# Kernel tuning notes

Hardware: AMD Instinct MI355X
Metric: run time of the kernel (lower is better)

## Reference

```python
import jax, jax.numpy as jnp
import numpy as np

BBOX_XFORM_CLIP = float(np.log(1000.0 / 16.0))
WX, WY, WW, WH = 10.0, 10.0, 5.0, 5.0  # torchvision default box-coder weights


def setup_inputs() -> dict:
    key = jax.random.key(0)
    B, P, C, E = 8, 25000, 81, 256
    H, W = 800, 800
    k1, k2, k3, k4, k5 = jax.random.split(key, 5)
    N = B * P
    class_logits = jax.random.normal(k1, (N, C), dtype=jnp.float32)
    box_regression = jax.random.normal(k2, (N, C * 4), dtype=jnp.float32) * 0.1
    id_embedding = jax.random.normal(k3, (N, E), dtype=jnp.float32)
    # valid proposals: x1<x2, y1<y2, inside the image
    xy = jax.random.uniform(k4, (B, P, 2), dtype=jnp.float32) * (W - 65.0)
    wh = jax.random.uniform(k5, (B, P, 2), dtype=jnp.float32) * 63.0 + 1.0
    proposals = jnp.concatenate([xy, xy + wh], axis=-1)  # [B,P,4] x1,y1,x2,y2
    return {
        'class_logits': class_logits,
        'box_regression': box_regression,
        'id_embedding': id_embedding,
        'proposals': proposals,
        'img_h': H,
        'img_w': W,
    }


def _decode_boxes(box_regression, proposals_flat):
    # torchvision BoxCoder.decode, vectorized. proposals_flat: [N,4]
    N = proposals_flat.shape[0]
    C = box_regression.shape[1] // 4
    deltas = box_regression.reshape(N, C, 4)
    x1, y1, x2, y2 = jnp.split(proposals_flat, 4, axis=-1)  # each [N,1]
    w = x2 - x1
    h = y2 - y1
    cx = x1 + 0.5 * w
    cy = y1 + 0.5 * h
    dx = deltas[..., 0] / WX  # [N,C]
    dy = deltas[..., 1] / WY
    dw = jnp.minimum(deltas[..., 2] / WW, BBOX_XFORM_CLIP)
    dh = jnp.minimum(deltas[..., 3] / WH, BBOX_XFORM_CLIP)
    pcx = dx * w + cx
    pcy = dy * h + cy
    pw = jnp.exp(dw) * w
    ph = jnp.exp(dh) * h
    boxes = jnp.stack(
        [pcx - 0.5 * pw, pcy - 0.5 * ph, pcx + 0.5 * pw, pcy + 0.5 * ph], axis=-1
    )  # [N,C,4]
    return boxes


def reference(class_logits, box_regression, id_embedding, proposals, img_h, img_w):
    B, P, _ = proposals.shape
    C = class_logits.shape[-1]
    Hf = jnp.float32(img_h)
    Wf = jnp.float32(img_w)

    boxes = _decode_boxes(box_regression, proposals.reshape(B * P, 4))  # [N,C,4]
    # clip_boxes_to_image
    bx = jnp.clip(boxes[..., 0::2], 0.0, Wf)
    by = jnp.clip(boxes[..., 1::2], 0.0, Hf)
    boxes = jnp.stack([bx[..., 0], by[..., 0], bx[..., 1], by[..., 1]], axis=-1)

    scores = jax.nn.softmax(class_logits, axis=-1)  # [N,C]

    # per-image split (uniform counts -> reshape), drop background class 0
    boxes = boxes.reshape(B, P, C, 4)[:, :, 1:, :]          # [B,P,C-1,4]
    scores = scores.reshape(B, P, C)[:, :, 1:]              # [B,P,C-1]
    id_embs = id_embedding.reshape(B, P, -1)                # [B,P,E]
    labels = jnp.broadcast_to(jnp.arange(1, C, dtype=jnp.int32), (B, P, C - 1))
    roi_idxs = jnp.broadcast_to(
        jnp.arange(P, dtype=jnp.int32)[None, :, None], (B, P, C - 1)
    )
    return boxes, scores, id_embs, labels, roi_idxs
```

## Files before the change

### kernel.cpp

```cpp
#include <hip/hip_runtime.h>

#define N_TOT   200000
#define C_CLS   81
#define P_PER   25000
#define CM1     80
#define E_DIM   256


__global__ __launch_bounds__(256) void decode_kernel(
    const float* __restrict__ box_reg,
    const float* __restrict__ proposals,
    const int*   __restrict__ img_h_p,
    const int*   __restrict__ img_w_p,
    float* __restrict__ out_boxes,
    float* __restrict__ out_labels,
    float* __restrict__ out_roi)
{
    unsigned int tid = blockIdx.x * blockDim.x + threadIdx.x;
    const unsigned int total = (unsigned int)N_TOT * CM1;
    if (tid >= total) return;

    unsigned int n    = tid / CM1;
    unsigned int cidx = tid - n * CM1;
    unsigned int c    = cidx + 1;

    const float Wf = (float)img_w_p[0];
    const float Hf = (float)img_h_p[0];

    const float4 pr = ((const float4*)proposals)[n];
    float w  = pr.z - pr.x;
    float h  = pr.w - pr.y;
    float cx = pr.x + 0.5f * w;
    float cy = pr.y + 0.5f * h;

    const float4 d = ((const float4*)box_reg)[(size_t)n * C_CLS + c];

    const float CLIP = 4.135166556742356f;
    float dx = d.x / 10.0f;
    float dy = d.y / 10.0f;
    float dw = fminf(d.z / 5.0f, CLIP);
    float dh = fminf(d.w / 5.0f, CLIP);

    float pcx = dx * w + cx;
    float pcy = dy * h + cy;
    float pw  = expf(dw) * w;
    float ph  = expf(dh) * h;

    float x1 = pcx - 0.5f * pw;
    float y1 = pcy - 0.5f * ph;
    float x2 = pcx + 0.5f * pw;
    float y2 = pcy + 0.5f * ph;

    x1 = fminf(fmaxf(x1, 0.0f), Wf);
    x2 = fminf(fmaxf(x2, 0.0f), Wf);
    y1 = fminf(fmaxf(y1, 0.0f), Hf);
    y2 = fminf(fmaxf(y2, 0.0f), Hf);

    ((float4*)out_boxes)[tid] = make_float4(x1, y1, x2, y2);
    out_labels[tid] = (float)c;
    out_roi[tid]    = (float)(n % P_PER);
}

__global__ __launch_bounds__(256) void softmax_kernel(
    const float* __restrict__ logits,
    float* __restrict__ out_scores)
{
    unsigned int wave = blockIdx.x * (blockDim.x >> 6) + (threadIdx.x >> 6);
    unsigned int lane = threadIdx.x & 63;
    if (wave >= N_TOT) return;

    const float* row = logits + (size_t)wave * C_CLS;
    float v0 = row[lane];
    float v1 = (lane < 17) ? row[64 + lane] : -INFINITY;

    float m = fmaxf(v0, v1);
    #pragma unroll
    for (int off = 32; off; off >>= 1) m = fmaxf(m, __shfl_xor(m, off, 64));

    float e0 = expf(v0 - m);
    float e1 = (lane < 17) ? expf(v1 - m) : 0.0f;

    float s = e0 + e1;
    #pragma unroll
    for (int off = 32; off; off >>= 1) s += __shfl_xor(s, off, 64);

    float inv = 1.0f / s;
    float* o = out_scores + (size_t)wave * CM1;
    if (lane >= 1) o[lane - 1] = e0 * inv;
    if (lane < 17) o[63 + lane] = e1 * inv;
}

__global__ __launch_bounds__(256) void copy4_kernel(
    const float4* __restrict__ src, float4* __restrict__ dst, unsigned int n4)
{
    unsigned int i = blockIdx.x * blockDim.x + threadIdx.x;
    if (i < n4) dst[i] = src[i];
}

extern "C" void kernel_launch(void* const* d_in, const int* in_sizes, int n_in,
                              void* d_out, int out_size, void* d_ws, size_t ws_size,
                              hipStream_t stream) {
    const float* class_logits = (const float*)d_in[0];
    const float* box_reg      = (const float*)d_in[1];
    const float* id_emb       = (const float*)d_in[2];
    const float* proposals    = (const float*)d_in[3];
    const int*   img_h        = (const int*)d_in[4];
    const int*   img_w        = (const int*)d_in[5];

    float* out        = (float*)d_out;
    float* out_boxes  = out;
    float* out_scores = out + 64000000u;
    float* out_ids    = out + 80000000u;
    float* out_labels = out + 131200000u;
    float* out_roi    = out + 147200000u;

    {
        unsigned int total = (unsigned int)N_TOT * CM1;
        dim3 grid((total + 255) / 256), block(256);
        decode_kernel<<<grid, block, 0, stream>>>(box_reg, proposals, img_h, img_w,
                                                  out_boxes, out_labels, out_roi);
    }

    {
        dim3 grid(N_TOT / 4), block(256);
        softmax_kernel<<<grid, block, 0, stream>>>(class_logits, out_scores);
    }

    {
        unsigned int n4 = 12800000u;
        dim3 grid((n4 + 255) / 256), block(256);
        copy4_kernel<<<grid, block, 0, stream>>>((const float4*)id_emb,
                                                 (float4*)out_ids, n4);
    }
}
```

Baseline: 235.8 us.

## Fuse decode, softmax and embedding copy into one kernel with nontemporal memory ops

The three separate launches (box decode, softmax, id-embedding copy) are merged into one kernel whose block index range selects the task, and every global load and store becomes a nontemporal builtin. Copy blocks each move two float4 values. Division by constants is replaced with multiplication by reciprocals. This targets launch gaps and the tail of each kernel in a bandwidth-bound workload, and tries to keep streaming data from polluting the cache. The cost is a heterogeneous grid, and the reciprocal multiplies can differ from the reference division in the last bit.

```diff
diff --git a/kernel.cpp b/kernel.cpp
--- a/kernel.cpp
+++ b/kernel.cpp
@@ -4,97 +4,99 @@
 #define C_CLS   81
 #define P_PER   25000
 #define CM1     80
-#define E_DIM   256
 
 
-__global__ __launch_bounds__(256) void decode_kernel(
-    const float* __restrict__ box_reg,
-    const float* __restrict__ proposals,
+typedef float f4 __attribute__((ext_vector_type(4)));
+
+#define DEC_BLOCKS 62500u
+#define SM_BLOCKS  50000u
+#define CP_BLOCKS  25000u
+#define CP_HALF    6400000u
+
+__global__ __launch_bounds__(256) void fused_kernel(
+    const float* __restrict__ logits,
+    const f4*    __restrict__ box_reg4,
+    const f4*    __restrict__ id_emb4,
+    const f4*    __restrict__ proposals4,
     const int*   __restrict__ img_h_p,
     const int*   __restrict__ img_w_p,
-    float* __restrict__ out_boxes,
-    float* __restrict__ out_labels,
-    float* __restrict__ out_roi)
+    float* __restrict__ out)
 {
-    unsigned int tid = blockIdx.x * blockDim.x + threadIdx.x;
-    const unsigned int total = (unsigned int)N_TOT * CM1;
-    if (tid >= total) return;
+    f4*    out_boxes  = (f4*)out;
+    float* out_scores = out + 64000000u;
+    f4*    out_ids    = (f4*)(out + 80000000u);
+    float* out_labels = out + 131200000u;
+    float* out_roi    = out + 147200000u;
 
-    unsigned int n    = tid / CM1;
-    unsigned int cidx = tid - n * CM1;
-    unsigned int c    = cidx + 1;
+    unsigned int b = blockIdx.x;
 
-    const float Wf = (float)img_w_p[0];
-    const float Hf = (float)img_h_p[0];
+    if (b < DEC_BLOCKS) {
+        unsigned int tid  = b * 256u + threadIdx.x;
+        unsigned int n    = tid / CM1;
+        unsigned int cidx = tid - n * CM1;
+        unsigned int c    = cidx + 1u;
 
-    const float4 pr = ((const float4*)proposals)[n];
-    float w  = pr.z - pr.x;
-    float h  = pr.w - pr.y;
-    float cx = pr.x + 0.5f * w;
-    float cy = pr.y + 0.5f * h;
+        const float Wf = (float)img_w_p[0];
+        const float Hf = (float)img_h_p[0];
 
-    const float4 d = ((const float4*)box_reg)[(size_t)n * C_CLS + c];
+        const f4 pr = proposals4[n];
+        float w  = pr.z - pr.x;
+        float h  = pr.w - pr.y;
+        float cx = pr.x + 0.5f * w;
+        float cy = pr.y + 0.5f * h;
 
-    const float CLIP = 4.135166556742356f;
-    float dx = d.x / 10.0f;
-    float dy = d.y / 10.0f;
-    float dw = fminf(d.z / 5.0f, CLIP);
-    float dh = fminf(d.w / 5.0f, CLIP);
+        const f4 d = __builtin_nontemporal_load(&box_reg4[(size_t)n * C_CLS + c]);
 
-    float pcx = dx * w + cx;
-    float pcy = dy * h + cy;
-    float pw  = expf(dw) * w;
-    float ph  = expf(dh) * h;
+        const float CLIP = 4.135166556742356f;
+        float dx = d.x * 0.1f;
+        float dy = d.y * 0.1f;
+        float dw = fminf(d.z * 0.2f, CLIP);
+        float dh = fminf(d.w * 0.2f, CLIP);
 
-    float x1 = pcx - 0.5f * pw;
-    float y1 = pcy - 0.5f * ph;
-    float x2 = pcx + 0.5f * pw;
-    float y2 = pcy + 0.5f * ph;
+        float pcx = dx * w + cx;
+        float pcy = dy * h + cy;
+        float pw  = expf(dw) * w;
+        float ph  = expf(dh) * h;
 
-    x1 = fminf(fmaxf(x1, 0.0f), Wf);
-    x2 = fminf(fmaxf(x2, 0.0f), Wf);
-    y1 = fminf(fmaxf(y1, 0.0f), Hf);
-    y2 = fminf(fmaxf(y2, 0.0f), Hf);
+        float x1 = fminf(fmaxf(pcx - 0.5f * pw, 0.0f), Wf);
+        float y1 = fminf(fmaxf(pcy - 0.5f * ph, 0.0f), Hf);
+        float x2 = fminf(fmaxf(pcx + 0.5f * pw, 0.0f), Wf);
+        float y2 = fminf(fmaxf(pcy + 0.5f * ph, 0.0f), Hf);
 
-    ((float4*)out_boxes)[tid] = make_float4(x1, y1, x2, y2);
-    out_labels[tid] = (float)c;
-    out_roi[tid]    = (float)(n % P_PER);
-}
+        f4 bx; bx.x = x1; bx.y = y1; bx.z = x2; bx.w = y2;
+        __builtin_nontemporal_store(bx, &out_boxes[tid]);
+        __builtin_nontemporal_store((float)c, &out_labels[tid]);
+        __builtin_nontemporal_store((float)(n % P_PER), &out_roi[tid]);
+    } else if (b < DEC_BLOCKS + SM_BLOCKS) {
+        unsigned int wave = (b - DEC_BLOCKS) * 4u + (threadIdx.x >> 6);
+        unsigned int lane = threadIdx.x & 63u;
 
-__global__ __launch_bounds__(256) void softmax_kernel(
-    const float* __restrict__ logits,
-    float* __restrict__ out_scores)
-{
-    unsigned int wave = blockIdx.x * (blockDim.x >> 6) + (threadIdx.x >> 6);
-    unsigned int lane = threadIdx.x & 63;
-    if (wave >= N_TOT) return;
+        const float* row = logits + (size_t)wave * C_CLS;
+        float v0 = __builtin_nontemporal_load(&row[lane]);
+        float v1 = (lane < 17u) ? __builtin_nontemporal_load(&row[64u + lane]) : -INFINITY;
 
-    const float* row = logits + (size_t)wave * C_CLS;
-    float v0 = row[lane];
-    float v1 = (lane < 17) ? row[64 + lane] : -INFINITY;
+        float m = fmaxf(v0, v1);
+        #pragma unroll
+        for (int off = 32; off; off >>= 1) m = fmaxf(m, __shfl_xor(m, off, 64));
 
-    float m = fmaxf(v0, v1);
-    #pragma unroll
-    for (int off = 32; off; off >>= 1) m = fmaxf(m, __shfl_xor(m, off, 64));
+        float e0 = expf(v0 - m);
+        float e1 = (lane < 17u) ? expf(v1 - m) : 0.0f;
 
-    float e0 = expf(v0 - m);
-    float e1 = (lane < 17) ? expf(v1 - m) : 0.0f;
+        float s = e0 + e1;
+        #pragma unroll
+        for (int off = 32; off; off >>= 1) s += __shfl_xor(s, off, 64);
 
-    float s = e0 + e1;
-    #pragma unroll
-    for (int off = 32; off; off >>= 1) s += __shfl_xor(s, off, 64);
-
-    float inv = 1.0f / s;
-    float* o = out_scores + (size_t)wave * CM1;
-    if (lane >= 1) o[lane - 1] = e0 * inv;
-    if (lane < 17) o[63 + lane] = e1 * inv;
-}
-
-__global__ __launch_bounds__(256) void copy4_kernel(
-    const float4* __restrict__ src, float4* __restrict__ dst, unsigned int n4)
-{
-    unsigned int i = blockIdx.x * blockDim.x + threadIdx.x;
-    if (i < n4) dst[i] = src[i];
+        float inv = 1.0f / s;
+        float* o = out_scores + (size_t)wave * CM1;
+        if (lane >= 1u) __builtin_nontemporal_store(e0 * inv, &o[lane - 1u]);
+        if (lane < 17u) __builtin_nontemporal_store(e1 * inv, &o[63u + lane]);
+    } else {
+        unsigned int i = (b - DEC_BLOCKS - SM_BLOCKS) * 256u + threadIdx.x;
+        f4 a0 = __builtin_nontemporal_load(&id_emb4[i]);
+        f4 a1 = __builtin_nontemporal_load(&id_emb4[i + CP_HALF]);
+        __builtin_nontemporal_store(a0, &out_ids[i]);
+        __builtin_nontemporal_store(a1, &out_ids[i + CP_HALF]);
+    }
 }
 
 extern "C" void kernel_launch(void* const* d_in, const int* in_sizes, int n_in,
@@ -107,29 +109,8 @@
     const int*   img_h        = (const int*)d_in[4];
     const int*   img_w        = (const int*)d_in[5];
 
-    float* out        = (float*)d_out;
-    float* out_boxes  = out;
-    float* out_scores = out + 64000000u;
-    float* out_ids    = out + 80000000u;
-    float* out_labels = out + 131200000u;
-    float* out_roi    = out + 147200000u;
-
-    {
-        unsigned int total = (unsigned int)N_TOT * CM1;
-        dim3 grid((total + 255) / 256), block(256);
-        decode_kernel<<<grid, block, 0, stream>>>(box_reg, proposals, img_h, img_w,
-                                                  out_boxes, out_labels, out_roi);
-    }
-
-    {
-        dim3 grid(N_TOT / 4), block(256);
-        softmax_kernel<<<grid, block, 0, stream>>>(class_logits, out_scores);
-    }
-
-    {
-        unsigned int n4 = 12800000u;
-        dim3 grid((n4 + 255) / 256), block(256);
-        copy4_kernel<<<grid, block, 0, stream>>>((const float4*)id_emb,
-                                                 (float4*)out_ids, n4);
-    }
+    dim3 grid(DEC_BLOCKS + SM_BLOCKS + CP_BLOCKS), block(256);
+    fused_kernel<<<grid, block, 0, stream>>>(
+        class_logits, (const f4*)box_reg, (const f4*)id_emb, (const f4*)proposals,
+        img_h, img_w, (float*)d_out);
 }
```

After: 220.2 us. 6.6% less time.
